# Kernel optimization log

Hardware: AMD Instinct MI355X
Metric: run time of the kernel (lower is better)

The kernel has to match this reference:

```python
import jax, jax.numpy as jnp
import numpy as np

B = 131072
HIDDEN = 256


def setup_inputs() -> dict:
    key = jax.random.key(0)
    ks = jax.random.split(key, 9)
    x = jax.random.uniform(ks[0], (B, 2), dtype=jnp.float32)
    # torch nn.Linear weights are [out_features, in_features]; kaiming-uniform-ish scale
    def w(k, out_f, in_f):
        bound = 1.0 / np.sqrt(in_f)
        return jax.random.uniform(k, (out_f, in_f), jnp.float32, -bound, bound)
    W0 = w(ks[1], HIDDEN, 2)
    W1 = w(ks[2], HIDDEN, HIDDEN)
    W2 = w(ks[3], HIDDEN, HIDDEN)
    W3 = w(ks[4], HIDDEN, HIDDEN)
    W4 = w(ks[5], HIDDEN, HIDDEN)
    W5 = w(ks[6], HIDDEN, HIDDEN)
    W6 = w(ks[7], HIDDEN, HIDDEN)
    W7 = w(ks[8], 3, HIDDEN)
    return {"x": x, "W0": W0, "W1": W1, "W2": W2, "W3": W3,
            "W4": W4, "W5": W5, "W6": W6, "W7": W7}


def reference(x, W0, W1, W2, W3, W4, W5, W6, W7):
    # 8 bias-free Linear layers: ReLU after layers 0..6, Sigmoid after layer 7.
    h = x
    for W in (W0, W1, W2, W3, W4, W5, W6):
        h = jax.nn.relu(h @ W.T)
    return jax.nn.sigmoid(h @ W7.T)  # [B, 3]
```

## Files before the change

kernel.cpp:

```cpp
#include <hip/hip_runtime.h>
#include <hip/hip_bf16.h>


#define HID 256
#define BM 128
#define NBLK 1024
#define HPITCH 264

typedef __attribute__((ext_vector_type(8))) short bf16x8;
typedef __attribute__((ext_vector_type(8))) unsigned short u16x8;
typedef __attribute__((ext_vector_type(4))) unsigned short u16x4;
typedef __attribute__((ext_vector_type(4))) float f32x4;
typedef __attribute__((ext_vector_type(16))) float f32x16;

__device__ __forceinline__ unsigned cvt_pk_bf16(float lo, float hi) {
    unsigned r;
    asm("v_cvt_pk_bf16_f32 %0, %1, %2" : "=v"(r) : "v"(lo), "v"(hi));
    return r;
}

struct WPtrs { const float* w[6]; const float* w7; };

__global__ void pack_w_kernel(WPtrs wp, unsigned short* __restrict__ Wp) {
    int tid = blockIdx.x * 256 + threadIdx.x;
    if (tid < 49152) {
        int l  = tid & 63;
        int ft = (tid >> 6) & 1;
        int kk = (tid >> 7) & 15;
        int fw = (tid >> 11) & 3;
        int L  = tid >> 13;
        int n  = 64 * fw + 32 * ft + (l & 31);
        int k0 = 16 * kk + 8 * (l >> 5);
        const float* src = wp.w[L] + n * HID + k0;
        u16x8 v;
#pragma unroll
        for (int j = 0; j < 8; ++j) {
            union { float f; unsigned u; } c; c.f = src[j];
            unsigned r = c.u + 0x7fffu + ((c.u >> 16) & 1u);
            v[j] = (unsigned short)(r >> 16);
        }
        *(u16x8*)(Wp + (size_t)tid * 8) = v;
    } else if (tid < 49664) {
        int t  = tid - 49152;
        int l  = t & 63;
        int kk = t >> 6;
        int n  = l & 15;
        int k0 = 32 * kk + 8 * (l >> 4);
        u16x8 v;
#pragma unroll
        for (int j = 0; j < 8; ++j) {
            unsigned short s = 0;
            if (n < 3) {
                union { float f; unsigned u; } c; c.f = wp.w7[n * HID + k0 + j];
                s = (unsigned short)((c.u + 0x7fffu + ((c.u >> 16) & 1u)) >> 16);
            }
            v[j] = s;
        }
        *(u16x8*)(Wp + 393216 + (size_t)t * 8) = v;
    }
}

__launch_bounds__(512, 4)
__global__ void mlp_fused_kernel(const float* __restrict__ x,
                                 const float* __restrict__ W0,
                                 const unsigned short* __restrict__ Wp,
                                 float* __restrict__ out) {
    __shared__ __align__(16) unsigned short Hs[BM][HPITCH];
    __shared__ __align__(16) float Ps[4][BM][4];
    __shared__ float xsf[2 * BM];

    const int tid = threadIdx.x;
    const int l   = tid & 63;
    const int w   = tid >> 6;
    const int fw  = w & 3;
    const int rb  = (w >> 2) * 64;
    const long r0 = (long)blockIdx.x * BM;

    const unsigned short* wbl = Wp + (size_t)fw * 16384 + (size_t)l * 8;

    bf16x8 wb[2][2];
    wb[0][0] = *(const bf16x8*)(wbl);
    wb[0][1] = *(const bf16x8*)(wbl + 512);

    if (tid < 2 * BM) xsf[tid] = x[r0 * 2 + tid];
    const int fp = (tid & 127) * 2;
    const int q  = tid >> 7;
    f32x4 w0v = *(const f32x4*)(W0 + 2 * fp);
    __syncthreads();

#pragma unroll
    for (int i = 0; i < 32; ++i) {
        int m = 32 * q + i;
        float x0 = xsf[2 * m], x1 = xsf[2 * m + 1];
        float ha = fmaf(x0, w0v[0], x1 * w0v[1]);
        float hb = fmaf(x0, w0v[2], x1 * w0v[3]);
        *(unsigned*)(&Hs[m][fp]) = cvt_pk_bf16(fmaxf(0.f, ha), fmaxf(0.f, hb));
    }
    __syncthreads();

    const int c  = l & 31;
    const int hi = l >> 5;
    for (int L = 0; L < 6; ++L) {
        f32x16 acc[2][2];
#pragma unroll
        for (int ft = 0; ft < 2; ++ft)
#pragma unroll
            for (int mt = 0; mt < 2; ++mt)
#pragma unroll
                for (int j = 0; j < 16; ++j) acc[ft][mt][j] = 0.f;

#pragma unroll
        for (int kk = 0; kk < 16; ++kk) {
            const int cur = kk & 1, nxt = cur ^ 1;
            if (kk < 15) {
                wb[nxt][0] = *(const bf16x8*)(wbl + L * 65536 + (kk + 1) * 1024);
                wb[nxt][1] = *(const bf16x8*)(wbl + L * 65536 + (kk + 1) * 1024 + 512);
            } else if (L < 5) {
                wb[nxt][0] = *(const bf16x8*)(wbl + (L + 1) * 65536);
                wb[nxt][1] = *(const bf16x8*)(wbl + (L + 1) * 65536 + 512);
            }
            bf16x8 a0 = *(const bf16x8*)(&Hs[rb + c][16 * kk + 8 * hi]);
            bf16x8 a1 = *(const bf16x8*)(&Hs[rb + 32 + c][16 * kk + 8 * hi]);
            acc[0][0] = __builtin_amdgcn_mfma_f32_32x32x16_bf16(wb[cur][0], a0, acc[0][0], 0, 0, 0);
            acc[0][1] = __builtin_amdgcn_mfma_f32_32x32x16_bf16(wb[cur][0], a1, acc[0][1], 0, 0, 0);
            acc[1][0] = __builtin_amdgcn_mfma_f32_32x32x16_bf16(wb[cur][1], a0, acc[1][0], 0, 0, 0);
            acc[1][1] = __builtin_amdgcn_mfma_f32_32x32x16_bf16(wb[cur][1], a1, acc[1][1], 0, 0, 0);
        }
        __syncthreads();
#pragma unroll
        for (int ft = 0; ft < 2; ++ft)
#pragma unroll
            for (int mt = 0; mt < 2; ++mt) {
                f32x16 v = acc[ft][mt];
#pragma unroll
                for (int g = 0; g < 4; ++g) {
                    union { unsigned u[2]; u16x4 s; } pk;
                    pk.u[0] = cvt_pk_bf16(fmaxf(0.f, v[4 * g]),     fmaxf(0.f, v[4 * g + 1]));
                    pk.u[1] = cvt_pk_bf16(fmaxf(0.f, v[4 * g + 2]), fmaxf(0.f, v[4 * g + 3]));
                    *(u16x4*)(&Hs[rb + 32 * mt + c][64 * fw + 32 * ft + 8 * g + 4 * hi]) = pk.s;
                }
            }
        __syncthreads();
    }

    const int lr = l & 15, lg = l >> 4;
    const unsigned short* w7b = Wp + 393216 + (size_t)l * 8;
    bf16x8 w7f0 = *(const bf16x8*)(w7b + (2 * fw) * 512);
    bf16x8 w7f1 = *(const bf16x8*)(w7b + (2 * fw + 1) * 512);
    f32x4 acc7[4];
#pragma unroll
    for (int mt = 0; mt < 4; ++mt) acc7[mt] = (f32x4){0.f, 0.f, 0.f, 0.f};
#pragma unroll
    for (int mt = 0; mt < 4; ++mt) {
        bf16x8 a = *(const bf16x8*)(&Hs[rb + 16 * mt + lr][32 * (2 * fw) + 8 * lg]);
        acc7[mt] = __builtin_amdgcn_mfma_f32_16x16x32_bf16(w7f0, a, acc7[mt], 0, 0, 0);
        bf16x8 b = *(const bf16x8*)(&Hs[rb + 16 * mt + lr][32 * (2 * fw + 1) + 8 * lg]);
        acc7[mt] = __builtin_amdgcn_mfma_f32_16x16x32_bf16(w7f1, b, acc7[mt], 0, 0, 0);
    }
    if (lg == 0) {
#pragma unroll
        for (int mt = 0; mt < 4; ++mt)
            *(f32x4*)(&Ps[fw][rb + 16 * mt + lr][0]) = acc7[mt];
    }
    __syncthreads();
    if (tid < 3 * BM) {
        int row = tid / 3, o = tid - 3 * row;
        float s = Ps[0][row][o] + Ps[1][row][o] + Ps[2][row][o] + Ps[3][row][o];
        out[r0 * 3 + tid] = 1.f / (1.f + __expf(-s));
    }
}

extern "C" void kernel_launch(void* const* d_in, const int* in_sizes, int n_in,
                              void* d_out, int out_size, void* d_ws, size_t ws_size,
                              hipStream_t stream) {
    const float* x  = (const float*)d_in[0];
    const float* W0 = (const float*)d_in[1];
    WPtrs wp;
    for (int i = 0; i < 6; ++i) wp.w[i] = (const float*)d_in[2 + i];
    wp.w7 = (const float*)d_in[8];
    float* out = (float*)d_out;
    unsigned short* Wp = (unsigned short*)d_ws;

    pack_w_kernel<<<194, 256, 0, stream>>>(wp, Wp);
    mlp_fused_kernel<<<NBLK, 512, 0, stream>>>(x, W0, Wp, out);
}
```

Before: 159.7 us.

## Double-buffer hidden activations in LDS and deepen weight prefetch to three stages

Result: slower. 170.7 us (+6.9%).

```diff
diff --git a/kernel.cpp b/kernel.cpp
--- a/kernel.cpp
+++ b/kernel.cpp
@@ -60,12 +60,12 @@
     }
 }
 
-__launch_bounds__(512, 4)
+__launch_bounds__(512, 1)
 __global__ void mlp_fused_kernel(const float* __restrict__ x,
                                  const float* __restrict__ W0,
                                  const unsigned short* __restrict__ Wp,
                                  float* __restrict__ out) {
-    __shared__ __align__(16) unsigned short Hs[BM][HPITCH];
+    __shared__ __align__(16) unsigned short Hs[2][BM][HPITCH];
     __shared__ __align__(16) float Ps[4][BM][4];
     __shared__ float xsf[2 * BM];
 
@@ -78,9 +78,15 @@
 
     const unsigned short* wbl = Wp + (size_t)fw * 16384 + (size_t)l * 8;
 
-    bf16x8 wb[2][2];
+    bf16x8 wb[3][2];
     wb[0][0] = *(const bf16x8*)(wbl);
     wb[0][1] = *(const bf16x8*)(wbl + 512);
+    wb[1][0] = *(const bf16x8*)(wbl + 1024);
+    wb[1][1] = *(const bf16x8*)(wbl + 1536);
+
+    const unsigned short* w7b = Wp + 393216 + (size_t)l * 8;
+    bf16x8 w7f0 = *(const bf16x8*)(w7b + (2 * fw) * 512);
+    bf16x8 w7f1 = *(const bf16x8*)(w7b + (2 * fw + 1) * 512);
 
     if (tid < 2 * BM) xsf[tid] = x[r0 * 2 + tid];
     const int fp = (tid & 127) * 2;
@@ -94,13 +100,15 @@
         float x0 = xsf[2 * m], x1 = xsf[2 * m + 1];
         float ha = fmaf(x0, w0v[0], x1 * w0v[1]);
         float hb = fmaf(x0, w0v[2], x1 * w0v[3]);
-        *(unsigned*)(&Hs[m][fp]) = cvt_pk_bf16(fmaxf(0.f, ha), fmaxf(0.f, hb));
+        *(unsigned*)(&Hs[0][m][fp]) = cvt_pk_bf16(fmaxf(0.f, ha), fmaxf(0.f, hb));
     }
     __syncthreads();
 
     const int c  = l & 31;
     const int hi = l >> 5;
+#pragma unroll
     for (int L = 0; L < 6; ++L) {
+        const int rp = L & 1, wp2 = rp ^ 1;
         f32x16 acc[2][2];
 #pragma unroll
         for (int ft = 0; ft < 2; ++ft)
@@ -111,50 +119,46 @@
 
 #pragma unroll
         for (int kk = 0; kk < 16; ++kk) {
-            const int cur = kk & 1, nxt = cur ^ 1;
-            if (kk < 15) {
-                wb[nxt][0] = *(const bf16x8*)(wbl + L * 65536 + (kk + 1) * 1024);
-                wb[nxt][1] = *(const bf16x8*)(wbl + L * 65536 + (kk + 1) * 1024 + 512);
-            } else if (L < 5) {
-                wb[nxt][0] = *(const bf16x8*)(wbl + (L + 1) * 65536);
-                wb[nxt][1] = *(const bf16x8*)(wbl + (L + 1) * 65536 + 512);
+            const int g   = 16 * L + kk;
+            const int cur = g % 3;
+            const int pre = (g + 2) % 3;
+            if (g + 2 < 96) {
+                const int gl = (g + 2) >> 4, gk = (g + 2) & 15;
+                wb[pre][0] = *(const bf16x8*)(wbl + gl * 65536 + gk * 1024);
+                wb[pre][1] = *(const bf16x8*)(wbl + gl * 65536 + gk * 1024 + 512);
             }
-            bf16x8 a0 = *(const bf16x8*)(&Hs[rb + c][16 * kk + 8 * hi]);
-            bf16x8 a1 = *(const bf16x8*)(&Hs[rb + 32 + c][16 * kk + 8 * hi]);
+            bf16x8 a0 = *(const bf16x8*)(&Hs[rp][rb + c][16 * kk + 8 * hi]);
+            bf16x8 a1 = *(const bf16x8*)(&Hs[rp][rb + 32 + c][16 * kk + 8 * hi]);
             acc[0][0] = __builtin_amdgcn_mfma_f32_32x32x16_bf16(wb[cur][0], a0, acc[0][0], 0, 0, 0);
             acc[0][1] = __builtin_amdgcn_mfma_f32_32x32x16_bf16(wb[cur][0], a1, acc[0][1], 0, 0, 0);
             acc[1][0] = __builtin_amdgcn_mfma_f32_32x32x16_bf16(wb[cur][1], a0, acc[1][0], 0, 0, 0);
             acc[1][1] = __builtin_amdgcn_mfma_f32_32x32x16_bf16(wb[cur][1], a1, acc[1][1], 0, 0, 0);
         }
-        __syncthreads();
 #pragma unroll
         for (int ft = 0; ft < 2; ++ft)
 #pragma unroll
             for (int mt = 0; mt < 2; ++mt) {
                 f32x16 v = acc[ft][mt];
 #pragma unroll
-                for (int g = 0; g < 4; ++g) {
+                for (int g2 = 0; g2 < 4; ++g2) {
                     union { unsigned u[2]; u16x4 s; } pk;
-                    pk.u[0] = cvt_pk_bf16(fmaxf(0.f, v[4 * g]),     fmaxf(0.f, v[4 * g + 1]));
-                    pk.u[1] = cvt_pk_bf16(fmaxf(0.f, v[4 * g + 2]), fmaxf(0.f, v[4 * g + 3]));
-                    *(u16x4*)(&Hs[rb + 32 * mt + c][64 * fw + 32 * ft + 8 * g + 4 * hi]) = pk.s;
+                    pk.u[0] = cvt_pk_bf16(fmaxf(0.f, v[4 * g2]),     fmaxf(0.f, v[4 * g2 + 1]));
+                    pk.u[1] = cvt_pk_bf16(fmaxf(0.f, v[4 * g2 + 2]), fmaxf(0.f, v[4 * g2 + 3]));
+                    *(u16x4*)(&Hs[wp2][rb + 32 * mt + c][64 * fw + 32 * ft + 8 * g2 + 4 * hi]) = pk.s;
                 }
             }
         __syncthreads();
     }
 
     const int lr = l & 15, lg = l >> 4;
-    const unsigned short* w7b = Wp + 393216 + (size_t)l * 8;
-    bf16x8 w7f0 = *(const bf16x8*)(w7b + (2 * fw) * 512);
-    bf16x8 w7f1 = *(const bf16x8*)(w7b + (2 * fw + 1) * 512);
     f32x4 acc7[4];
 #pragma unroll
     for (int mt = 0; mt < 4; ++mt) acc7[mt] = (f32x4){0.f, 0.f, 0.f, 0.f};
 #pragma unroll
     for (int mt = 0; mt < 4; ++mt) {
-        bf16x8 a = *(const bf16x8*)(&Hs[rb + 16 * mt + lr][32 * (2 * fw) + 8 * lg]);
+        bf16x8 a = *(const bf16x8*)(&Hs[0][rb + 16 * mt + lr][32 * (2 * fw) + 8 * lg]);
         acc7[mt] = __builtin_amdgcn_mfma_f32_16x16x32_bf16(w7f0, a, acc7[mt], 0, 0, 0);
-        bf16x8 b = *(const bf16x8*)(&Hs[rb + 16 * mt + lr][32 * (2 * fw + 1) + 8 * lg]);
+        bf16x8 b = *(const bf16x8*)(&Hs[0][rb + 16 * mt + lr][32 * (2 * fw + 1) + 8 * lg]);
         acc7[mt] = __builtin_amdgcn_mfma_f32_16x16x32_bf16(w7f1, b, acc7[mt], 0, 0, 0);
     }
     if (lg == 0) {
```

## Keep activations in registers per wave, removing shared-memory staging between layers

Applied to the files above, without the earlier changes.

After: 373.1 us. +133.7%, slower.

```diff
diff --git a/kernel.cpp b/kernel.cpp
--- a/kernel.cpp
+++ b/kernel.cpp
@@ -3,14 +3,12 @@
 
 
 #define HID 256
-#define BM 128
-#define NBLK 1024
-#define HPITCH 264
 
 typedef __attribute__((ext_vector_type(8))) short bf16x8;
 typedef __attribute__((ext_vector_type(8))) unsigned short u16x8;
-typedef __attribute__((ext_vector_type(4))) unsigned short u16x4;
+typedef __attribute__((ext_vector_type(4))) unsigned u32x4;
 typedef __attribute__((ext_vector_type(4))) float f32x4;
+typedef __attribute__((ext_vector_type(2))) float f32x2;
 typedef __attribute__((ext_vector_type(16))) float f32x16;
 
 __device__ __forceinline__ unsigned cvt_pk_bf16(float lo, float hi) {
@@ -18,8 +16,14 @@
     asm("v_cvt_pk_bf16_f32 %0, %1, %2" : "=v"(r) : "v"(lo), "v"(hi));
     return r;
 }
+__device__ __forceinline__ float bf_lo(unsigned u) {
+    union { unsigned u; float f; } v; v.u = u << 16; return v.f;
+}
+__device__ __forceinline__ float bf_hi(unsigned u) {
+    union { unsigned u; float f; } v; v.u = u & 0xffff0000u; return v.f;
+}
 
-struct WPtrs { const float* w[6]; const float* w7; };
+struct WPtrs { const float* w[6]; const float* w0; const float* w7; };
 
 __global__ void pack_w_kernel(WPtrs wp, unsigned short* __restrict__ Wp) {
     int tid = blockIdx.x * 256 + threadIdx.x;
@@ -30,157 +34,133 @@
         int fw = (tid >> 11) & 3;
         int L  = tid >> 13;
         int n  = 64 * fw + 32 * ft + (l & 31);
-        int k0 = 16 * kk + 8 * (l >> 5);
-        const float* src = wp.w[L] + n * HID + k0;
+        const float* src = wp.w[L] + n * HID + 16 * kk + 4 * (l >> 5);
         u16x8 v;
 #pragma unroll
         for (int j = 0; j < 8; ++j) {
-            union { float f; unsigned u; } c; c.f = src[j];
+            union { float f; unsigned u; } c; c.f = src[8 * (j >> 2) + (j & 3)];
             unsigned r = c.u + 0x7fffu + ((c.u >> 16) & 1u);
             v[j] = (unsigned short)(r >> 16);
         }
         *(u16x8*)(Wp + (size_t)tid * 8) = v;
+    } else if (tid < 49408) {
+        int t  = tid - 49152;
+        int hi = t >> 7, kk = (t >> 3) & 15, s = t & 7;
+        int f  = 16 * kk + 8 * (s >> 2) + 4 * hi + (s & 3);
+        float* dst = (float*)((char*)Wp + 786432) + (size_t)t * 4;
+        dst[0] = wp.w7[0 * HID + f];
+        dst[1] = wp.w7[1 * HID + f];
+        dst[2] = wp.w7[2 * HID + f];
+        dst[3] = 0.f;
     } else if (tid < 49664) {
-        int t  = tid - 49152;
-        int l  = t & 63;
-        int kk = t >> 6;
-        int n  = l & 15;
-        int k0 = 32 * kk + 8 * (l >> 4);
-        u16x8 v;
-#pragma unroll
-        for (int j = 0; j < 8; ++j) {
-            unsigned short s = 0;
-            if (n < 3) {
-                union { float f; unsigned u; } c; c.f = wp.w7[n * HID + k0 + j];
-                s = (unsigned short)((c.u + 0x7fffu + ((c.u >> 16) & 1u)) >> 16);
-            }
-            v[j] = s;
-        }
-        *(u16x8*)(Wp + 393216 + (size_t)t * 8) = v;
+        int t  = tid - 49408;
+        int hi = t >> 7, kk = (t >> 3) & 15, s = t & 7;
+        int f  = 16 * kk + 8 * (s >> 2) + 4 * hi + (s & 3);
+        float* dst = (float*)((char*)Wp + 790528) + (size_t)t * 2;
+        dst[0] = wp.w0[2 * f];
+        dst[1] = wp.w0[2 * f + 1];
     }
 }
 
-__launch_bounds__(512, 4)
+template<int LBASE>
+__device__ __forceinline__ void layer_body(const unsigned short* wlane,
+                                           const u32x4* IN, u32x4* OUT) {
+#pragma unroll
+    for (int C = 0; C < 8; ++C) {
+        f32x16 acc;
+#pragma unroll
+        for (int j = 0; j < 16; ++j) acc[j] = 0.f;
+#pragma unroll
+        for (int kk = 0; kk < 16; ++kk) {
+            const int fidx = (((C >> 1) * 16 + kk) * 2 + (C & 1));
+            bf16x8 wf = *(const bf16x8*)(wlane + (size_t)LBASE * 65536 + fidx * 512);
+            bf16x8 af = *(const bf16x8*)(&IN[kk]);
+            acc = __builtin_amdgcn_mfma_f32_32x32x16_bf16(wf, af, acc, 0, 0, 0);
+        }
+        u32x4 o0, o1;
+#pragma unroll
+        for (int t = 0; t < 4; ++t) {
+            o0[t] = cvt_pk_bf16(fmaxf(0.f, acc[2 * t]),     fmaxf(0.f, acc[2 * t + 1]));
+            o1[t] = cvt_pk_bf16(fmaxf(0.f, acc[8 + 2 * t]), fmaxf(0.f, acc[8 + 2 * t + 1]));
+        }
+        OUT[2 * C]     = o0;
+        OUT[2 * C + 1] = o1;
+    }
+}
+
+__launch_bounds__(256, 2)
 __global__ void mlp_fused_kernel(const float* __restrict__ x,
-                                 const float* __restrict__ W0,
                                  const unsigned short* __restrict__ Wp,
                                  float* __restrict__ out) {
-    __shared__ __align__(16) unsigned short Hs[BM][HPITCH];
-    __shared__ __align__(16) float Ps[4][BM][4];
-    __shared__ float xsf[2 * BM];
-
     const int tid = threadIdx.x;
     const int l   = tid & 63;
-    const int w   = tid >> 6;
-    const int fw  = w & 3;
-    const int rb  = (w >> 2) * 64;
-    const long r0 = (long)blockIdx.x * BM;
+    const int wv  = tid >> 6;
+    const int hi  = l >> 5;
+    const long row = (long)blockIdx.x * 128 + wv * 32 + (l & 31);
 
-    const unsigned short* wbl = Wp + (size_t)fw * 16384 + (size_t)l * 8;
+    const unsigned short* wlane = Wp + (size_t)l * 8;
 
-    bf16x8 wb[2][2];
-    wb[0][0] = *(const bf16x8*)(wbl);
-    wb[0][1] = *(const bf16x8*)(wbl + 512);
-
-    if (tid < 2 * BM) xsf[tid] = x[r0 * 2 + tid];
-    const int fp = (tid & 127) * 2;
-    const int q  = tid >> 7;
-    f32x4 w0v = *(const f32x4*)(W0 + 2 * fp);
-    __syncthreads();
-
+    f32x2 xv = *(const f32x2*)(x + row * 2);
+    const float* w0p = (const float*)((const char*)Wp + 790528) + hi * 256;
+    u32x4 U[16], O[16];
 #pragma unroll
-    for (int i = 0; i < 32; ++i) {
-        int m = 32 * q + i;
-        float x0 = xsf[2 * m], x1 = xsf[2 * m + 1];
-        float ha = fmaf(x0, w0v[0], x1 * w0v[1]);
-        float hb = fmaf(x0, w0v[2], x1 * w0v[3]);
-        *(unsigned*)(&Hs[m][fp]) = cvt_pk_bf16(fmaxf(0.f, ha), fmaxf(0.f, hb));
-    }
-    __syncthreads();
-
-    const int c  = l & 31;
-    const int hi = l >> 5;
-    for (int L = 0; L < 6; ++L) {
-        f32x16 acc[2][2];
+    for (int kk = 0; kk < 16; ++kk) {
+        u32x4 g;
 #pragma unroll
-        for (int ft = 0; ft < 2; ++ft)
-#pragma unroll
-            for (int mt = 0; mt < 2; ++mt)
-#pragma unroll
-                for (int j = 0; j < 16; ++j) acc[ft][mt][j] = 0.f;
-
-#pragma unroll
-        for (int kk = 0; kk < 16; ++kk) {
-            const int cur = kk & 1, nxt = cur ^ 1;
-            if (kk < 15) {
-                wb[nxt][0] = *(const bf16x8*)(wbl + L * 65536 + (kk + 1) * 1024);
-                wb[nxt][1] = *(const bf16x8*)(wbl + L * 65536 + (kk + 1) * 1024 + 512);
-            } else if (L < 5) {
-                wb[nxt][0] = *(const bf16x8*)(wbl + (L + 1) * 65536);
-                wb[nxt][1] = *(const bf16x8*)(wbl + (L + 1) * 65536 + 512);
-            }
-            bf16x8 a0 = *(const bf16x8*)(&Hs[rb + c][16 * kk + 8 * hi]);
-            bf16x8 a1 = *(const bf16x8*)(&Hs[rb + 32 + c][16 * kk + 8 * hi]);
-            acc[0][0] = __builtin_amdgcn_mfma_f32_32x32x16_bf16(wb[cur][0], a0, acc[0][0], 0, 0, 0);
-            acc[0][1] = __builtin_amdgcn_mfma_f32_32x32x16_bf16(wb[cur][0], a1, acc[0][1], 0, 0, 0);
-            acc[1][0] = __builtin_amdgcn_mfma_f32_32x32x16_bf16(wb[cur][1], a0, acc[1][0], 0, 0, 0);
-            acc[1][1] = __builtin_amdgcn_mfma_f32_32x32x16_bf16(wb[cur][1], a1, acc[1][1], 0, 0, 0);
+        for (int t = 0; t < 4; ++t) {
+            f32x4 wq = *(const f32x4*)(w0p + kk * 16 + 4 * t);
+            float h0 = fmaf(xv[0], wq[0], xv[1] * wq[1]);
+            float h1 = fmaf(xv[0], wq[2], xv[1] * wq[3]);
+            g[t] = cvt_pk_bf16(fmaxf(0.f, h0), fmaxf(0.f, h1));
         }
-        __syncthreads();
-#pragma unroll
-        for (int ft = 0; ft < 2; ++ft)
-#pragma unroll
-            for (int mt = 0; mt < 2; ++mt) {
-                f32x16 v = acc[ft][mt];
-#pragma unroll
-                for (int g = 0; g < 4; ++g) {
-                    union { unsigned u[2]; u16x4 s; } pk;
-                    pk.u[0] = cvt_pk_bf16(fmaxf(0.f, v[4 * g]),     fmaxf(0.f, v[4 * g + 1]));
-                    pk.u[1] = cvt_pk_bf16(fmaxf(0.f, v[4 * g + 2]), fmaxf(0.f, v[4 * g + 3]));
-                    *(u16x4*)(&Hs[rb + 32 * mt + c][64 * fw + 32 * ft + 8 * g + 4 * hi]) = pk.s;
-                }
-            }
-        __syncthreads();
+        U[kk] = g;
     }
 
-    const int lr = l & 15, lg = l >> 4;
-    const unsigned short* w7b = Wp + 393216 + (size_t)l * 8;
-    bf16x8 w7f0 = *(const bf16x8*)(w7b + (2 * fw) * 512);
-    bf16x8 w7f1 = *(const bf16x8*)(w7b + (2 * fw + 1) * 512);
-    f32x4 acc7[4];
+    layer_body<0>(wlane, U, O);
+    layer_body<1>(wlane, O, U);
+    layer_body<2>(wlane, U, O);
+    layer_body<3>(wlane, O, U);
+    layer_body<4>(wlane, U, O);
+    layer_body<5>(wlane, O, U);
+
+    const float* w7p = (const float*)((const char*)Wp + 786432) + hi * 512;
+    float a0 = 0.f, a1 = 0.f, a2 = 0.f;
 #pragma unroll
-    for (int mt = 0; mt < 4; ++mt) acc7[mt] = (f32x4){0.f, 0.f, 0.f, 0.f};
+    for (int kk = 0; kk < 16; ++kk) {
+        u32x4 g = U[kk];
 #pragma unroll
-    for (int mt = 0; mt < 4; ++mt) {
-        bf16x8 a = *(const bf16x8*)(&Hs[rb + 16 * mt + lr][32 * (2 * fw) + 8 * lg]);
-        acc7[mt] = __builtin_amdgcn_mfma_f32_16x16x32_bf16(w7f0, a, acc7[mt], 0, 0, 0);
-        bf16x8 b = *(const bf16x8*)(&Hs[rb + 16 * mt + lr][32 * (2 * fw + 1) + 8 * lg]);
-        acc7[mt] = __builtin_amdgcn_mfma_f32_16x16x32_bf16(w7f1, b, acc7[mt], 0, 0, 0);
+        for (int idx = 0; idx < 4; ++idx) {
+            unsigned u = g[idx];
+            float hlo = bf_lo(u), hhi = bf_hi(u);
+            f32x4 wA = *(const f32x4*)(w7p + (kk * 8 + 2 * idx) * 4);
+            f32x4 wB = *(const f32x4*)(w7p + (kk * 8 + 2 * idx + 1) * 4);
+            a0 = fmaf(hlo, wA[0], fmaf(hhi, wB[0], a0));
+            a1 = fmaf(hlo, wA[1], fmaf(hhi, wB[1], a1));
+            a2 = fmaf(hlo, wA[2], fmaf(hhi, wB[2], a2));
+        }
     }
-    if (lg == 0) {
-#pragma unroll
-        for (int mt = 0; mt < 4; ++mt)
-            *(f32x4*)(&Ps[fw][rb + 16 * mt + lr][0]) = acc7[mt];
-    }
-    __syncthreads();
-    if (tid < 3 * BM) {
-        int row = tid / 3, o = tid - 3 * row;
-        float s = Ps[0][row][o] + Ps[1][row][o] + Ps[2][row][o] + Ps[3][row][o];
-        out[r0 * 3 + tid] = 1.f / (1.f + __expf(-s));
+    a0 += __shfl_xor(a0, 32);
+    a1 += __shfl_xor(a1, 32);
+    a2 += __shfl_xor(a2, 32);
+    if (l < 32) {
+        long o = row * 3;
+        out[o + 0] = 1.f / (1.f + __expf(-a0));
+        out[o + 1] = 1.f / (1.f + __expf(-a1));
+        out[o + 2] = 1.f / (1.f + __expf(-a2));
     }
 }
 
 extern "C" void kernel_launch(void* const* d_in, const int* in_sizes, int n_in,
                               void* d_out, int out_size, void* d_ws, size_t ws_size,
                               hipStream_t stream) {
-    const float* x  = (const float*)d_in[0];
-    const float* W0 = (const float*)d_in[1];
+    const float* x = (const float*)d_in[0];
     WPtrs wp;
+    wp.w0 = (const float*)d_in[1];
     for (int i = 0; i < 6; ++i) wp.w[i] = (const float*)d_in[2 + i];
     wp.w7 = (const float*)d_in[8];
     float* out = (float*)d_out;
     unsigned short* Wp = (unsigned short*)d_ws;
 
     pack_w_kernel<<<194, 256, 0, stream>>>(wp, Wp);
-    mlp_fused_kernel<<<NBLK, 512, 0, stream>>>(x, W0, Wp, out);
+    mlp_fused_kernel<<<1024, 256, 0, stream>>>(x, Wp, out);
 }
```
